# Performance work log

Measured on AMD Instinct MI355X. Metric: run time of the kernel, lower is better.

The kernel has to match this reference:

```python
import jax, jax.numpy as jnp
import numpy as np
from jax import lax


def avg_pool3(x):
    # F.avg_pool2d(x, 3, 1, 1) with count_include_pad=True: zero-pad, divide by 9.
    s = lax.reduce_window(x, 0.0, lax.add, (1, 1, 3, 3), (1, 1, 1, 1),
                          [(0, 0), (0, 0), (1, 1), (1, 1)])
    return s / 9.0


def resize_bilinear_ac(x, H, W):
    # bilinear resize with align_corners=True, separable gathers
    B, C, h, w = x.shape
    if (h, w) == (H, W):
        return x
    yc = jnp.linspace(0.0, h - 1.0, H)
    xc = jnp.linspace(0.0, w - 1.0, W)
    y0 = jnp.floor(yc).astype(jnp.int32); y1 = jnp.minimum(y0 + 1, h - 1)
    x0 = jnp.floor(xc).astype(jnp.int32); x1 = jnp.minimum(x0 + 1, w - 1)
    wy = (yc - y0).astype(x.dtype)
    wx = (xc - x0).astype(x.dtype)
    xr = x[:, :, y0, :] * (1.0 - wy)[None, None, :, None] + x[:, :, y1, :] * wy[None, None, :, None]
    return xr[:, :, :, x0] * (1.0 - wx) + xr[:, :, :, x1] * wx


def grid_sample_border(img, grid):
    # F.grid_sample(mode='bilinear', padding_mode='border', align_corners=True)
    B, C, H, W = img.shape
    x = jnp.clip((grid[..., 0] + 1.0) * 0.5 * (W - 1), 0.0, W - 1.0)
    y = jnp.clip((grid[..., 1] + 1.0) * 0.5 * (H - 1), 0.0, H - 1.0)
    x0 = jnp.floor(x).astype(jnp.int32); y0 = jnp.floor(y).astype(jnp.int32)
    x1 = jnp.minimum(x0 + 1, W - 1); y1 = jnp.minimum(y0 + 1, H - 1)
    wx = (x - x0)[..., None]; wy = (y - y0)[..., None]
    imt = jnp.transpose(img, (0, 2, 3, 1))  # [B,H,W,C]
    b = jnp.arange(B)[:, None, None]
    v00 = imt[b, y0, x0]; v01 = imt[b, y0, x1]
    v10 = imt[b, y1, x0]; v11 = imt[b, y1, x1]
    top = v00 * (1.0 - wx) + v01 * wx
    bot = v10 * (1.0 - wx) + v11 * wx
    out = top * (1.0 - wy) + bot * wy
    return jnp.transpose(out, (0, 3, 1, 2))


def warp_image(img, flow):
    B, C, H, W = img.shape
    _, _, h, w = flow.shape
    flow = resize_bilinear_ac(flow, H, W)
    scale = jnp.array([W / w, H / h], dtype=img.dtype).reshape(1, 2, 1, 1)
    flow = flow * scale
    yy, xx = jnp.meshgrid(jnp.linspace(-1.0, 1.0, H, dtype=img.dtype),
                          jnp.linspace(-1.0, 1.0, W, dtype=img.dtype), indexing='ij')
    base = jnp.stack((xx, yy), axis=-1)[None]  # [1,H,W,2]
    fn = jnp.stack([2.0 * flow[:, 0] / max(W - 1, 1),
                    2.0 * flow[:, 1] / max(H - 1, 1)], axis=-1)  # [B,H,W,2]
    return grid_sample_border(img, base + fn)


def ssim_map(x, y, C1=0.01 ** 2, C2=0.03 ** 2):
    mu_x = avg_pool3(x); mu_y = avg_pool3(y)
    sigma_x = avg_pool3(x * x) - mu_x * mu_x
    sigma_y = avg_pool3(y * y) - mu_y * mu_y
    sigma_xy = avg_pool3(x * y) - mu_x * mu_y
    ssim = (2 * mu_x * mu_y + C1) * (2 * sigma_xy + C2) / \
           ((mu_x ** 2 + mu_y ** 2 + C1) * (sigma_x + sigma_y + C2) + 1e-12)
    return jnp.mean(jnp.clip((1.0 - ssim) / 2.0, 0.0, 1.0), axis=1, keepdims=True)


def masked_mean(x, mask):
    m = (mask > 0.5).astype(x.dtype)
    num = jnp.sum(x * m)
    den = jnp.maximum(jnp.sum(m), 1.0)
    return num / den


def smoothness_loss(flow):
    dx = jnp.abs(flow[:, :, :, :-1] - flow[:, :, :, 1:])
    dy = jnp.abs(flow[:, :, :-1, :] - flow[:, :, 1:, :])
    return jnp.mean(dx) + jnp.mean(dy)


def setup_inputs() -> dict:
    key = jax.random.key(0)
    k1, k2, k3, k4 = jax.random.split(key, 4)
    B, H, W = 8, 512, 1024
    h, w = 128, 256
    return {
        'flow': jax.random.normal(k1, (B, 2, h, w), dtype=jnp.float32),
        'img1': jax.random.uniform(k2, (B, 3, H, W), dtype=jnp.float32),
        'img2': jax.random.uniform(k3, (B, 3, H, W), dtype=jnp.float32),
        'valid_mask': jax.random.uniform(k4, (B, 1, H, W), dtype=jnp.float32),
    }


def reference(flow, img1, img2, valid_mask):
    alpha_photo, alpha_smooth = 1.0, 0.1
    img2_warp = warp_image(img2, flow)
    l1 = jnp.mean(jnp.abs(img1 - img2_warp), axis=1, keepdims=True)
    photo_map = 0.85 * ssim_map(img1, img2_warp) + 0.15 * l1
    photo = masked_mean(photo_map, valid_mask)
    smooth = smoothness_loss(flow)
    total = alpha_photo * photo + alpha_smooth * smooth
    return (total, photo, smooth)
```

## Files before the change

### kernel.cpp

```cpp
#include <hip/hip_runtime.h>

#define B_   8
#define H_   512
#define W_   1024
#define FH_  128
#define FW_  256
#define TW   64
#define TH   16
#define HW_  (TW + 2)
#define HH_  (TH + 2)
#define NSLOT 256

__device__ __forceinline__ float wave_reduce(float v) {
    #pragma unroll
    for (int off = 32; off > 0; off >>= 1) v += __shfl_down(v, off, 64);
    return v;
}

__device__ __forceinline__ void hrow(const float* __restrict__ a, const float* __restrict__ b,
                                     float& hA, float& hB, float& hAA, float& hBB, float& hAB) {
    const float a0 = a[0], a1 = a[1], a2 = a[2];
    const float b0 = b[0], b1 = b[1], b2 = b[2];
    hA  = a0 + a1 + a2;
    hB  = b0 + b1 + b2;
    hAA = fmaf(a0, a0, fmaf(a1, a1, a2 * a2));
    hBB = fmaf(b0, b0, fmaf(b1, b1, b2 * b2));
    hAB = fmaf(a0, b0, fmaf(a1, b1, a2 * b2));
}

__global__ __launch_bounds__(256)
void fused_main(const float* __restrict__ flow, const float* __restrict__ img1,
                const float* __restrict__ img2, const float* __restrict__ mask,
                float* __restrict__ accum) {
    const int b   = blockIdx.z;
    const int tx0 = blockIdx.x * TW;
    const int ty0 = blockIdx.y * TH;
    const int tid = threadIdx.x;

    __shared__ float s1[3][HH_][HW_];
    __shared__ float s2[3][HH_][HW_];

    const uint32_t plane = (uint32_t)H_ * W_;
    const float* f0  = flow + (size_t)b * 2 * FH_ * FW_;
    const float* f1  = f0 + FH_ * FW_;
    const float* i10 = img1 + (size_t)b * 3 * plane;
    const float* i11 = i10 + plane;
    const float* i12 = i11 + plane;
    const float* i20 = img2 + (size_t)b * 3 * plane;
    const float* i21 = i20 + plane;
    const float* i22 = i21 + plane;

    for (int i = tid; i < HH_ * HW_; i += 256) {
        const int ly = i / HW_;
        const int lx = i - ly * HW_;
        const int gy = ty0 + ly - 1;
        const int gx = tx0 + lx - 1;
        float v10 = 0.f, v11 = 0.f, v12 = 0.f;
        float v20 = 0.f, v21 = 0.f, v22 = 0.f;
        if (gy >= 0 && gy < H_ && gx >= 0 && gx < W_) {
            const uint32_t p = (uint32_t)gy * W_ + (uint32_t)gx;
            v10 = i10[p]; v11 = i11[p]; v12 = i12[p];

            const float yc = gy * (127.0f / 511.0f);
            const float xc = gx * (255.0f / 1023.0f);
            const int y0 = (int)yc, x0 = (int)xc;
            const int y1i = min(y0 + 1, FH_ - 1);
            const int x1i = min(x0 + 1, FW_ - 1);
            const float wy = yc - (float)y0, wx = xc - (float)x0;
            const uint32_t r0 = (uint32_t)y0 * FW_;
            const uint32_t r1 = (uint32_t)y1i * FW_;
            const float a00 = f0[r0 + x0], a01 = f0[r0 + x1i];
            const float a10 = f0[r1 + x0], a11 = f0[r1 + x1i];
            const float c00 = f1[r0 + x0], c01 = f1[r0 + x1i];
            const float c10 = f1[r1 + x0], c11 = f1[r1 + x1i];
            const float fxt = a00 + wx * (a01 - a00);
            const float fxb = a10 + wx * (a11 - a10);
            const float fx  = fxt + wy * (fxb - fxt);
            const float fyt = c00 + wx * (c01 - c00);
            const float fyb = c10 + wx * (c11 - c10);
            const float fy  = fyt + wy * (fyb - fyt);

            const float gxs = fminf(fmaxf(fmaf(4.0f, fx, (float)gx), 0.0f), (float)(W_ - 1));
            const float gys = fminf(fmaxf(fmaf(4.0f, fy, (float)gy), 0.0f), (float)(H_ - 1));
            const int sx0 = (int)gxs, sy0 = (int)gys;
            const int sx1 = min(sx0 + 1, W_ - 1);
            const int sy1 = min(sy0 + 1, H_ - 1);
            const float swx = gxs - (float)sx0, swy = gys - (float)sy0;
            const uint32_t p00 = (uint32_t)sy0 * W_ + (uint32_t)sx0;
            const uint32_t p01 = (uint32_t)sy0 * W_ + (uint32_t)sx1;
            const uint32_t p10 = (uint32_t)sy1 * W_ + (uint32_t)sx0;
            const uint32_t p11 = (uint32_t)sy1 * W_ + (uint32_t)sx1;

            {
                const float t = i20[p00] + swx * (i20[p01] - i20[p00]);
                const float u = i20[p10] + swx * (i20[p11] - i20[p10]);
                v20 = t + swy * (u - t);
            }
            {
                const float t = i21[p00] + swx * (i21[p01] - i21[p00]);
                const float u = i21[p10] + swx * (i21[p11] - i21[p10]);
                v21 = t + swy * (u - t);
            }
            {
                const float t = i22[p00] + swx * (i22[p01] - i22[p00]);
                const float u = i22[p10] + swx * (i22[p11] - i22[p10]);
                v22 = t + swy * (u - t);
            }
        }
        s1[0][ly][lx] = v10; s1[1][ly][lx] = v11; s1[2][ly][lx] = v12;
        s2[0][ly][lx] = v20; s2[1][ly][lx] = v21; s2[2][ly][lx] = v22;
    }

    const int lx  = tid & 63;
    const int lyg = tid >> 6;
    const int rb  = lyg * 4;
    const float* mb = mask + (size_t)b * plane;
    const uint32_t mb0 = (uint32_t)(ty0 + rb) * W_ + (uint32_t)(tx0 + lx);
    float mreg[4];
    #pragma unroll
    for (int k = 0; k < 4; ++k) mreg[k] = mb[mb0 + (uint32_t)k * W_];

    __syncthreads();

    const float inv9 = 1.0f / 9.0f;
    const float C1 = 0.0001f, C2 = 0.0009f;
    float dist[4] = {0.f, 0.f, 0.f, 0.f};
    float l1s [4] = {0.f, 0.f, 0.f, 0.f};

    #pragma unroll
    for (int c = 0; c < 3; ++c) {
        float hA0,hB0,hAA0,hBB0,hAB0;
        float hA1,hB1,hAA1,hBB1,hAB1;
        float hA2,hB2,hAA2,hBB2,hAB2;
        hrow(&s1[c][rb + 0][lx], &s2[c][rb + 0][lx], hA0,hB0,hAA0,hBB0,hAB0);
        hrow(&s1[c][rb + 1][lx], &s2[c][rb + 1][lx], hA1,hB1,hAA1,hBB1,hAB1);
        #pragma unroll
        for (int k = 0; k < 4; ++k) {
            hrow(&s1[c][rb + k + 2][lx], &s2[c][rb + k + 2][lx], hA2,hB2,hAA2,hBB2,hAB2);
            const float sA  = hA0  + hA1  + hA2;
            const float sB  = hB0  + hB1  + hB2;
            const float sAA = hAA0 + hAA1 + hAA2;
            const float sBB = hBB0 + hBB1 + hBB2;
            const float sAB = hAB0 + hAB1 + hAB2;
            const float mx  = sA * inv9, my = sB * inv9;
            const float vx  = fmaf(-mx, mx, sAA * inv9);
            const float vy  = fmaf(-my, my, sBB * inv9);
            const float vxy = fmaf(-mx, my, sAB * inv9);
            const float numt = (2.f * mx * my + C1) * (2.f * vxy + C2);
            const float dent = fmaf(fmaf(mx, mx, fmaf(my, my, C1)), (vx + vy + C2), 1e-12f);
            const float ssim = numt * __builtin_amdgcn_rcpf(dent);
            dist[k] += fminf(fmaxf((1.0f - ssim) * 0.5f, 0.f), 1.f);
            const float ac = s1[c][rb + k + 1][lx + 1];
            const float bc = s2[c][rb + k + 1][lx + 1];
            l1s[k] += fabsf(ac - bc);
            hA0 = hA1; hB0 = hB1; hAA0 = hAA1; hBB0 = hBB1; hAB0 = hAB1;
            hA1 = hA2; hB1 = hB2; hAA1 = hAA2; hBB1 = hBB2; hAB1 = hAB2;
        }
    }

    float num_acc = 0.f, den_acc = 0.f;
    #pragma unroll
    for (int k = 0; k < 4; ++k) {
        const float pmv = 0.28333334f * dist[k] + 0.05f * l1s[k];
        const float m   = (mreg[k] > 0.5f) ? 1.f : 0.f;
        num_acc = fmaf(pmv, m, num_acc);
        den_acc += m;
    }

    float num = wave_reduce(num_acc);
    float den = wave_reduce(den_acc);
    __shared__ float rn[4], rd[4];
    const int wid = tid >> 6, lane = tid & 63;
    if (lane == 0) { rn[wid] = num; rd[wid] = den; }
    __syncthreads();
    if (tid == 0) {
        const int lin = (blockIdx.z * gridDim.y + blockIdx.y) * gridDim.x + blockIdx.x;
        float* slot = accum + (size_t)(lin & (NSLOT - 1)) * 4;
        atomicAdd(&slot[0], rn[0] + rn[1] + rn[2] + rn[3]);
        atomicAdd(&slot[1], rd[0] + rd[1] + rd[2] + rd[3]);
    }
}

__global__ __launch_bounds__(256)
void smooth_kernel(const float* __restrict__ flow, float* __restrict__ accum) {
    const int N = B_ * 2 * FH_ * FW_;
    float dxs = 0.f, dys = 0.f;
    for (int i = blockIdx.x * 256 + threadIdx.x; i < N; i += gridDim.x * 256) {
        const float f = flow[i];
        const int x = i & (FW_ - 1);
        const int y = (i >> 8) & (FH_ - 1);
        if (x < FW_ - 1) dxs += fabsf(f - flow[i + 1]);
        if (y < FH_ - 1) dys += fabsf(f - flow[i + FW_]);
    }
    dxs = wave_reduce(dxs);
    dys = wave_reduce(dys);
    __shared__ float rn[4], rd[4];
    const int wid = threadIdx.x >> 6, lane = threadIdx.x & 63;
    if (lane == 0) { rn[wid] = dxs; rd[wid] = dys; }
    __syncthreads();
    if (threadIdx.x == 0) {
        float* slot = accum + (size_t)blockIdx.x * 4;
        atomicAdd(&slot[2], rn[0] + rn[1] + rn[2] + rn[3]);
        atomicAdd(&slot[3], rd[0] + rd[1] + rd[2] + rd[3]);
    }
}

__global__ __launch_bounds__(256)
void finalize_kernel(const float* __restrict__ accum, float* __restrict__ out) {
    const int t = threadIdx.x;
    float num = accum[t * 4 + 0];
    float den = accum[t * 4 + 1];
    float dxs = accum[t * 4 + 2];
    float dys = accum[t * 4 + 3];
    num = wave_reduce(num); den = wave_reduce(den);
    dxs = wave_reduce(dxs); dys = wave_reduce(dys);
    __shared__ float r[4][4];
    const int wid = t >> 6, lane = t & 63;
    if (lane == 0) { r[wid][0] = num; r[wid][1] = den; r[wid][2] = dxs; r[wid][3] = dys; }
    __syncthreads();
    if (t == 0) {
        const float tn = r[0][0] + r[1][0] + r[2][0] + r[3][0];
        const float td = r[0][1] + r[1][1] + r[2][1] + r[3][1];
        const float tx = r[0][2] + r[1][2] + r[2][2] + r[3][2];
        const float ty = r[0][3] + r[1][3] + r[2][3] + r[3][3];
        const float photo   = tn / fmaxf(td, 1.0f);
        const float mean_dx = tx / (float)(B_ * 2 * FH_ * (FW_ - 1));
        const float mean_dy = ty / (float)(B_ * 2 * (FH_ - 1) * FW_);
        const float smooth  = mean_dx + mean_dy;
        out[0] = photo + 0.1f * smooth;
        out[1] = photo;
        out[2] = smooth;
    }
}

extern "C" void kernel_launch(void* const* d_in, const int* in_sizes, int n_in,
                              void* d_out, int out_size, void* d_ws, size_t ws_size,
                              hipStream_t stream) {
    const float* flow = (const float*)d_in[0];
    const float* img1 = (const float*)d_in[1];
    const float* img2 = (const float*)d_in[2];
    const float* mask = (const float*)d_in[3];
    float* out   = (float*)d_out;
    float* accum = (float*)d_ws;

    hipMemsetAsync(accum, 0, NSLOT * 4 * sizeof(float), stream);
    smooth_kernel<<<NSLOT, 256, 0, stream>>>(flow, accum);
    dim3 grid(W_ / TW, H_ / TH, B_);
    fused_main<<<grid, 256, 0, stream>>>(flow, img1, img2, mask, accum);
    finalize_kernel<<<1, 256, 0, stream>>>(accum, out);
}
```

Baseline: 204.7 us.

## Stage flow in LDS, pack halo as half2, swizzle blocks, raise occupancy

The flow bilinear taps now come from a small per-block LDS tile instead of eight global loads per pixel. The img1/img2 halo is stored as packed half2 in LDS, which halves shared memory and the number of LDS reads. Blocks are remapped from a 1D grid, which plausibly spreads batches across XCDs or L2 slices, and launch bounds request 5 blocks per CU. The half-precision staging adds rounding error to the SSIM statistics, and the new stages add an extra __syncthreads.

```diff
diff --git a/kernel.cpp b/kernel.cpp
--- a/kernel.cpp
+++ b/kernel.cpp
@@ -1,4 +1,5 @@
 #include <hip/hip_runtime.h>
+#include <hip/hip_fp16.h>
 
 #define B_   8
 #define H_   512
@@ -9,6 +10,9 @@
 #define TH   16
 #define HW_  (TW + 2)
 #define HH_  (TH + 2)
+#define NHALO (HH_ * HW_)
+#define FR_  8
+#define FC_  20
 #define NSLOT 256
 
 __device__ __forceinline__ float wave_reduce(float v) {
@@ -17,28 +21,32 @@
     return v;
 }
 
-__device__ __forceinline__ void hrow(const float* __restrict__ a, const float* __restrict__ b,
+__device__ __forceinline__ void hrow(const __half2* __restrict__ s,
                                      float& hA, float& hB, float& hAA, float& hBB, float& hAB) {
-    const float a0 = a[0], a1 = a[1], a2 = a[2];
-    const float b0 = b[0], b1 = b[1], b2 = b[2];
-    hA  = a0 + a1 + a2;
-    hB  = b0 + b1 + b2;
-    hAA = fmaf(a0, a0, fmaf(a1, a1, a2 * a2));
-    hBB = fmaf(b0, b0, fmaf(b1, b1, b2 * b2));
-    hAB = fmaf(a0, b0, fmaf(a1, b1, a2 * b2));
-}
-
-__global__ __launch_bounds__(256)
+    const float2 p0 = __half22float2(s[0]);
+    const float2 p1 = __half22float2(s[1]);
+    const float2 p2 = __half22float2(s[2]);
+    hA  = p0.x + p1.x + p2.x;
+    hB  = p0.y + p1.y + p2.y;
+    hAA = fmaf(p0.x, p0.x, fmaf(p1.x, p1.x, p2.x * p2.x));
+    hBB = fmaf(p0.y, p0.y, fmaf(p1.y, p1.y, p2.y * p2.y));
+    hAB = fmaf(p0.x, p0.y, fmaf(p1.x, p1.y, p2.x * p2.y));
+}
+
+__global__ __launch_bounds__(256, 5)
 void fused_main(const float* __restrict__ flow, const float* __restrict__ img1,
                 const float* __restrict__ img2, const float* __restrict__ mask,
                 float* __restrict__ accum) {
-    const int b   = blockIdx.z;
-    const int tx0 = blockIdx.x * TW;
-    const int ty0 = blockIdx.y * TH;
+    const int bid = blockIdx.x;
+    const int lin = (bid & 7) * 512 + (bid >> 3);
+    const int b   = lin >> 9;
+    const int rem = lin & 511;
+    const int ty0 = (rem >> 4) * TH;
+    const int tx0 = (rem & 15) * TW;
     const int tid = threadIdx.x;
 
-    __shared__ float s1[3][HH_][HW_];
-    __shared__ float s2[3][HH_][HW_];
+    __shared__ __half2 sP[3][HH_][HW_];
+    __shared__ float   sF[2][FR_][FC_];
 
     const uint32_t plane = (uint32_t)H_ * W_;
     const float* f0  = flow + (size_t)b * 2 * FH_ * FW_;
@@ -50,65 +58,18 @@
     const float* i21 = i20 + plane;
     const float* i22 = i21 + plane;
 
-    for (int i = tid; i < HH_ * HW_; i += 256) {
-        const int ly = i / HW_;
-        const int lx = i - ly * HW_;
-        const int gy = ty0 + ly - 1;
-        const int gx = tx0 + lx - 1;
-        float v10 = 0.f, v11 = 0.f, v12 = 0.f;
-        float v20 = 0.f, v21 = 0.f, v22 = 0.f;
-        if (gy >= 0 && gy < H_ && gx >= 0 && gx < W_) {
-            const uint32_t p = (uint32_t)gy * W_ + (uint32_t)gx;
-            v10 = i10[p]; v11 = i11[p]; v12 = i12[p];
-
-            const float yc = gy * (127.0f / 511.0f);
-            const float xc = gx * (255.0f / 1023.0f);
-            const int y0 = (int)yc, x0 = (int)xc;
-            const int y1i = min(y0 + 1, FH_ - 1);
-            const int x1i = min(x0 + 1, FW_ - 1);
-            const float wy = yc - (float)y0, wx = xc - (float)x0;
-            const uint32_t r0 = (uint32_t)y0 * FW_;
-            const uint32_t r1 = (uint32_t)y1i * FW_;
-            const float a00 = f0[r0 + x0], a01 = f0[r0 + x1i];
-            const float a10 = f0[r1 + x0], a11 = f0[r1 + x1i];
-            const float c00 = f1[r0 + x0], c01 = f1[r0 + x1i];
-            const float c10 = f1[r1 + x0], c11 = f1[r1 + x1i];
-            const float fxt = a00 + wx * (a01 - a00);
-            const float fxb = a10 + wx * (a11 - a10);
-            const float fx  = fxt + wy * (fxb - fxt);
-            const float fyt = c00 + wx * (c01 - c00);
-            const float fyb = c10 + wx * (c11 - c10);
-            const float fy  = fyt + wy * (fyb - fyt);
-
-            const float gxs = fminf(fmaxf(fmaf(4.0f, fx, (float)gx), 0.0f), (float)(W_ - 1));
-            const float gys = fminf(fmaxf(fmaf(4.0f, fy, (float)gy), 0.0f), (float)(H_ - 1));
-            const int sx0 = (int)gxs, sy0 = (int)gys;
-            const int sx1 = min(sx0 + 1, W_ - 1);
-            const int sy1 = min(sy0 + 1, H_ - 1);
-            const float swx = gxs - (float)sx0, swy = gys - (float)sy0;
-            const uint32_t p00 = (uint32_t)sy0 * W_ + (uint32_t)sx0;
-            const uint32_t p01 = (uint32_t)sy0 * W_ + (uint32_t)sx1;
-            const uint32_t p10 = (uint32_t)sy1 * W_ + (uint32_t)sx0;
-            const uint32_t p11 = (uint32_t)sy1 * W_ + (uint32_t)sx1;
-
-            {
-                const float t = i20[p00] + swx * (i20[p01] - i20[p00]);
-                const float u = i20[p10] + swx * (i20[p11] - i20[p10]);
-                v20 = t + swy * (u - t);
-            }
-            {
-                const float t = i21[p00] + swx * (i21[p01] - i21[p00]);
-                const float u = i21[p10] + swx * (i21[p11] - i21[p10]);
-                v21 = t + swy * (u - t);
-            }
-            {
-                const float t = i22[p00] + swx * (i22[p01] - i22[p00]);
-                const float u = i22[p10] + swx * (i22[p11] - i22[p10]);
-                v22 = t + swy * (u - t);
-            }
-        }
-        s1[0][ly][lx] = v10; s1[1][ly][lx] = v11; s1[2][ly][lx] = v12;
-        s2[0][ly][lx] = v20; s2[1][ly][lx] = v21; s2[2][ly][lx] = v22;
+    const int fx0s = (tx0 > 0) ? (int)((float)(tx0 - 1) * (255.0f / 1023.0f)) : 0;
+    const int fy0s = (ty0 > 0) ? (int)((float)(ty0 - 1) * (127.0f / 511.0f)) : 0;
+    if (tid < 2 * FR_ * FC_ - 256 || tid < 256) {
+    }
+    for (int i = tid; i < 2 * FR_ * FC_; i += 256) {
+        const int ch = i / (FR_ * FC_);
+        const int r  = (i - ch * FR_ * FC_) / FC_;
+        const int cc = i - ch * FR_ * FC_ - r * FC_;
+        const int sy = min(fy0s + r, FH_ - 1);
+        const int sx = min(fx0s + cc, FW_ - 1);
+        const float* fp = ch ? f1 : f0;
+        sF[ch][r][cc] = fp[(uint32_t)sy * FW_ + (uint32_t)sx];
     }
 
     const int lx  = tid & 63;
@@ -122,6 +83,70 @@
 
     __syncthreads();
 
+    #pragma unroll
+    for (int s = 0; s < 5; ++s) {
+        const int i = tid + s * 256;
+        if (i < NHALO) {
+            const int ly = i / HW_;
+            const int lxh = i - ly * HW_;
+            const int gy = ty0 + ly - 1;
+            const int gx = tx0 + lxh - 1;
+            float v10 = 0.f, v11 = 0.f, v12 = 0.f;
+            float v20 = 0.f, v21 = 0.f, v22 = 0.f;
+            if (gy >= 0 && gy < H_ && gx >= 0 && gx < W_) {
+                const uint32_t p = (uint32_t)gy * W_ + (uint32_t)gx;
+                v10 = i10[p]; v11 = i11[p]; v12 = i12[p];
+
+                const float yc = gy * (127.0f / 511.0f);
+                const float xc = gx * (255.0f / 1023.0f);
+                const int y0 = (int)yc, x0 = (int)xc;
+                const float wy = yc - (float)y0, wx = xc - (float)x0;
+                const int yr = y0 - fy0s, xr = x0 - fx0s;
+                const float a00 = sF[0][yr][xr],     a01 = sF[0][yr][xr + 1];
+                const float a10 = sF[0][yr + 1][xr], a11 = sF[0][yr + 1][xr + 1];
+                const float c00 = sF[1][yr][xr],     c01 = sF[1][yr][xr + 1];
+                const float c10 = sF[1][yr + 1][xr], c11 = sF[1][yr + 1][xr + 1];
+                const float fxt = a00 + wx * (a01 - a00);
+                const float fxb = a10 + wx * (a11 - a10);
+                const float fx  = fxt + wy * (fxb - fxt);
+                const float fyt = c00 + wx * (c01 - c00);
+                const float fyb = c10 + wx * (c11 - c10);
+                const float fy  = fyt + wy * (fyb - fyt);
+
+                const float gxs = fminf(fmaxf(fmaf(4.0f, fx, (float)gx), 0.0f), (float)(W_ - 1));
+                const float gys = fminf(fmaxf(fmaf(4.0f, fy, (float)gy), 0.0f), (float)(H_ - 1));
+                const int sx0 = (int)gxs, sy0 = (int)gys;
+                const int sx1 = min(sx0 + 1, W_ - 1);
+                const int sy1 = min(sy0 + 1, H_ - 1);
+                const float swx = gxs - (float)sx0, swy = gys - (float)sy0;
+                const uint32_t p00 = (uint32_t)sy0 * W_ + (uint32_t)sx0;
+                const uint32_t p01 = (uint32_t)sy0 * W_ + (uint32_t)sx1;
+                const uint32_t p10 = (uint32_t)sy1 * W_ + (uint32_t)sx0;
+                const uint32_t p11 = (uint32_t)sy1 * W_ + (uint32_t)sx1;
+                {
+                    const float t = i20[p00] + swx * (i20[p01] - i20[p00]);
+                    const float u = i20[p10] + swx * (i20[p11] - i20[p10]);
+                    v20 = t + swy * (u - t);
+                }
+                {
+                    const float t = i21[p00] + swx * (i21[p01] - i21[p00]);
+                    const float u = i21[p10] + swx * (i21[p11] - i21[p10]);
+                    v21 = t + swy * (u - t);
+                }
+                {
+                    const float t = i22[p00] + swx * (i22[p01] - i22[p00]);
+                    const float u = i22[p10] + swx * (i22[p11] - i22[p10]);
+                    v22 = t + swy * (u - t);
+                }
+            }
+            sP[0][ly][lxh] = __floats2half2_rn(v10, v20);
+            sP[1][ly][lxh] = __floats2half2_rn(v11, v21);
+            sP[2][ly][lxh] = __floats2half2_rn(v12, v22);
+        }
+    }
+
+    __syncthreads();
+
     const float inv9 = 1.0f / 9.0f;
     const float C1 = 0.0001f, C2 = 0.0009f;
     float dist[4] = {0.f, 0.f, 0.f, 0.f};
@@ -132,11 +157,11 @@
         float hA0,hB0,hAA0,hBB0,hAB0;
         float hA1,hB1,hAA1,hBB1,hAB1;
         float hA2,hB2,hAA2,hBB2,hAB2;
-        hrow(&s1[c][rb + 0][lx], &s2[c][rb + 0][lx], hA0,hB0,hAA0,hBB0,hAB0);
-        hrow(&s1[c][rb + 1][lx], &s2[c][rb + 1][lx], hA1,hB1,hAA1,hBB1,hAB1);
+        hrow(&sP[c][rb + 0][lx], hA0,hB0,hAA0,hBB0,hAB0);
+        hrow(&sP[c][rb + 1][lx], hA1,hB1,hAA1,hBB1,hAB1);
         #pragma unroll
         for (int k = 0; k < 4; ++k) {
-            hrow(&s1[c][rb + k + 2][lx], &s2[c][rb + k + 2][lx], hA2,hB2,hAA2,hBB2,hAB2);
+            hrow(&sP[c][rb + k + 2][lx], hA2,hB2,hAA2,hBB2,hAB2);
             const float sA  = hA0  + hA1  + hA2;
             const float sB  = hB0  + hB1  + hB2;
             const float sAA = hAA0 + hAA1 + hAA2;
@@ -150,9 +175,8 @@
             const float dent = fmaf(fmaf(mx, mx, fmaf(my, my, C1)), (vx + vy + C2), 1e-12f);
             const float ssim = numt * __builtin_amdgcn_rcpf(dent);
             dist[k] += fminf(fmaxf((1.0f - ssim) * 0.5f, 0.f), 1.f);
-            const float ac = s1[c][rb + k + 1][lx + 1];
-            const float bc = s2[c][rb + k + 1][lx + 1];
-            l1s[k] += fabsf(ac - bc);
+            const float2 ctr = __half22float2(sP[c][rb + k + 1][lx + 1]);
+            l1s[k] += fabsf(ctr.x - ctr.y);
             hA0 = hA1; hB0 = hB1; hAA0 = hAA1; hBB0 = hBB1; hAB0 = hAB1;
             hA1 = hA2; hB1 = hB2; hAA1 = hAA2; hBB1 = hBB2; hAB1 = hAB2;
         }
@@ -174,8 +198,7 @@
     if (lane == 0) { rn[wid] = num; rd[wid] = den; }
     __syncthreads();
     if (tid == 0) {
-        const int lin = (blockIdx.z * gridDim.y + blockIdx.y) * gridDim.x + blockIdx.x;
-        float* slot = accum + (size_t)(lin & (NSLOT - 1)) * 4;
+        float* slot = accum + (size_t)(bid & (NSLOT - 1)) * 4;
         atomicAdd(&slot[0], rn[0] + rn[1] + rn[2] + rn[3]);
         atomicAdd(&slot[1], rd[0] + rd[1] + rd[2] + rd[3]);
     }
@@ -245,7 +268,6 @@
 
     hipMemsetAsync(accum, 0, NSLOT * 4 * sizeof(float), stream);
     smooth_kernel<<<NSLOT, 256, 0, stream>>>(flow, accum);
-    dim3 grid(W_ / TW, H_ / TH, B_);
-    fused_main<<<grid, 256, 0, stream>>>(flow, img1, img2, mask, accum);
+    fused_main<<<(W_ / TW) * (H_ / TH) * B_, 256, 0, stream>>>(flow, img1, img2, mask, accum);
     finalize_kernel<<<1, 256, 0, stream>>>(accum, out);
 }
```

Result: faster. 196.0 us (-4.3%).
